# Kernel tuning notes

Hardware: AMD Instinct MI355X
Metric: run time of the kernel (lower is better)

The kernel has to match this reference:

```python
import jax, jax.numpy as jnp
import numpy as np

VOCAB, VEC, HID, ATT, DOM, B, S = 50000, 300, 256, 500, 16, 64, 128


def _gru_scan(gi_all, h0, Whh, bhh):
    # gi_all: [S,B,3H] precomputed input projections; returns hs: [S,B,H]
    def step(h, gi):
        gh = h @ Whh.T + bhh
        i_r, i_z, i_n = jnp.split(gi, 3, axis=-1)
        h_r, h_z, h_n = jnp.split(gh, 3, axis=-1)
        r = jax.nn.sigmoid(i_r + h_r)
        zg = jax.nn.sigmoid(i_z + h_z)
        n = jnp.tanh(i_n + r * h_n)
        h_new = (1.0 - zg) * n + zg * h
        return h_new, h_new
    _, hs = jax.lax.scan(step, h0, gi_all)
    return hs


def setup_inputs() -> dict:
    key = jax.random.key(0)
    ks = jax.random.split(key, 16)
    def xavier(k, shape):
        fan_in, fan_out = shape[-1], shape[0]
        std = float(np.sqrt(2.0 / (fan_in + fan_out)))
        return jax.random.normal(k, shape, dtype=jnp.float32) * std
    inp = {
        'x': jax.random.randint(ks[0], (B, S), 0, VOCAB),
        'z': jax.random.randint(ks[1], (B,), 0, DOM),
        'emb': jax.random.normal(ks[2], (VOCAB, VEC), dtype=jnp.float32) * 0.1,
        'Wih_f': xavier(ks[3], (3 * HID, VEC)),
        'Whh_f': xavier(ks[4], (3 * HID, HID)),
        'bih_f': jnp.zeros((3 * HID,), jnp.float32),
        'bhh_f': jnp.zeros((3 * HID,), jnp.float32),
        'Wih_b': xavier(ks[5], (3 * HID, VEC)),
        'Whh_b': xavier(ks[6], (3 * HID, HID)),
        'bih_b': jnp.zeros((3 * HID,), jnp.float32),
        'bhh_b': jnp.zeros((3 * HID,), jnp.float32),
        'att_fc_W': xavier(ks[7], (ATT, 2 * HID)),
        'att_fc_b': jnp.zeros((ATT,), jnp.float32),
        'att_weight': xavier(ks[8], (DOM, ATT)),
        'fc_W': xavier(ks[9], (2, 2 * HID)),
        'fc_b': jnp.zeros((2,), jnp.float32),
    }
    return inp


def reference(x, z, emb, Wih_f, Whh_f, bih_f, bhh_f, Wih_b, Whh_b, bih_b, bhh_b,
              att_fc_W, att_fc_b, att_weight, fc_W, fc_b):
    xe = emb[x]                              # [B,S,VEC]
    xs = jnp.transpose(xe, (1, 0, 2))        # [S,B,VEC] (seq-major like torch GRU)
    h0 = jnp.zeros((x.shape[0], HID), jnp.float32)
    gi_f = jnp.einsum('sbv,gv->sbg', xs, Wih_f) + bih_f
    hs_f = _gru_scan(gi_f, h0, Whh_f, bhh_f)                       # [S,B,H]
    gi_b = jnp.einsum('sbv,gv->sbg', xs[::-1], Wih_b) + bih_b
    hs_b = _gru_scan(gi_b, h0, Whh_b, bhh_b)[::-1]                 # [S,B,H]
    h = jnp.transpose(jnp.concatenate([hs_f, hs_b], axis=-1), (1, 0, 2))  # [B,S,2H]
    hr = jnp.tanh(jnp.einsum('bsh,ah->bsa', h, att_fc_W) + att_fc_b)      # [B,S,ATT]
    # batched gather of per-domain attention vector, then per-row dot
    u = jnp.einsum('bsa,ba->bs', hr, att_weight[z])                        # [B,S]
    att = jax.nn.softmax(u, axis=1)                                        # [B,S]
    pooled = jnp.einsum('bsh,bs->bh', h, att)                              # [B,2H]
    # dropout is identity in eval mode
    return pooled @ fc_W.T + fc_b                                          # [B,2]
```

## Files before the change

kernel.cpp:

```cpp
#include <hip/hip_runtime.h>
#include <math.h>

#define VEC   300
#define HID   256
#define ATT   500
#define NB    64
#define NS    128
#define G3    768
#define GIC   1536
#define H2    512

typedef _Float16 half1;
typedef _Float16 h2_t  __attribute__((ext_vector_type(2)));
typedef _Float16 f16x8 __attribute__((ext_vector_type(8)));
typedef float    f32x4 __attribute__((ext_vector_type(4)));

struct __align__(16) H8 { h2_t a, b, c, d; };

#if __has_builtin(__builtin_amdgcn_exp2f)
#define EXP2F(x) __builtin_amdgcn_exp2f(x)
#else
#define EXP2F(x) exp2f(x)
#endif
#if __has_builtin(__builtin_amdgcn_rcpf)
#define RCPF(x) __builtin_amdgcn_rcpf(x)
#else
#define RCPF(x) (1.0f/(x))
#endif

__device__ __forceinline__ float sigm(float x){ return RCPF(1.f + EXP2F(-1.44269504f*x)); }
__device__ __forceinline__ float tanh_fast(float x){ return 1.f - 2.f*RCPF(1.f + EXP2F(2.88539008f*x)); }

#if __has_builtin(__builtin_amdgcn_fdot2)
#define FDOT(w,h,acc) __builtin_amdgcn_fdot2((w),(h),(acc),false)
#else
#define FDOT(w,h,acc) ((acc) + (float)(w).x*(float)(h).x + (float)(w).y*(float)(h).y)
#endif

__global__ __launch_bounds__(256) void k_prep(const float* __restrict__ Wf,
                       const float* __restrict__ Wb, h2_t* __restrict__ Wpk){
  int o = blockIdx.x*256 + threadIdx.x;
  int t = o & 1023;
  int rest = o >> 10;
  int j = rest % 3;
  int p = (rest/3) & 31;
  int dir = rest / 96;
  int u = t & 255, ks = t >> 8;
  const float* W = dir ? Wb : Wf;
  int k0 = ks*64 + 2*p;
  h2_t w;
  w.x = (half1)W[(j*HID+u)*HID + k0];
  w.y = (half1)W[(j*HID+u)*HID + k0 + 1];
  Wpk[o] = w;
}

__global__ __launch_bounds__(256) void k_prepA(const float* __restrict__ afW,
                       half1* __restrict__ afW16){
  int o = blockIdx.x*256 + threadIdx.x;
  int n = o >> 9, k = o & 511;
  afW16[o] = (half1)((n < ATT) ? afW[n*H2 + k] : 0.f);
}

__global__ __launch_bounds__(256)
__attribute__((amdgpu_waves_per_eu(4, 4)))
void k_gi_mfma(const int* __restrict__ x,
      const float* __restrict__ emb,
      const float* __restrict__ Wf, const float* __restrict__ Wb,
      const float* __restrict__ bf, const float* __restrict__ bb,
      float* __restrict__ gi){
  __shared__ half1 Al[128*40];
  __shared__ half1 Bl[128*40];
  __shared__ int   xi[128];
  const int t = threadIdx.x;
  const int row0 = blockIdx.x * 128;
  const int col0 = blockIdx.y * 128;
  if (t < 128) {
    int i = row0 + t; int s = i >> 6; int b = i & 63;
    xi[t] = x[b*NS + s];
  }
  __syncthreads();

  const int lane = t & 63, wid = t >> 6;
  const int wr = wid >> 1, wc = wid & 1;
  const int l15 = lane & 15, lk = lane >> 4;

  f32x4 acc[4][4];
#pragma unroll
  for (int i = 0; i < 4; ++i)
#pragma unroll
    for (int j = 0; j < 4; ++j) acc[i][j] = (f32x4){0.f,0.f,0.f,0.f};

  for (int ks = 0; ks < 10; ++ks) {
#pragma unroll
    for (int l = 0; l < 8; ++l) {
      int idx = l*256 + t;
      int row = idx >> 4;
      int kp  = idx & 15;
      int kk  = ks*32 + kp*2;
      h2_t va; va.x = (half1)0.f; va.y = (half1)0.f;
      h2_t vb; vb.x = (half1)0.f; vb.y = (half1)0.f;
      if (kk < VEC) {
        float2 e = *reinterpret_cast<const float2*>(&emb[(long)xi[row]*VEC + kk]);
        va.x = (half1)e.x; va.y = (half1)e.y;
        int g = col0 + row;
        const float* W = (g < G3) ? &Wf[(long)g*VEC] : &Wb[(long)(g-G3)*VEC];
        float2 w2 = *reinterpret_cast<const float2*>(&W[kk]);
        vb.x = (half1)w2.x; vb.y = (half1)w2.y;
      }
      *reinterpret_cast<h2_t*>(&Al[row*40 + kp*2]) = va;
      *reinterpret_cast<h2_t*>(&Bl[row*40 + kp*2]) = vb;
    }
    __syncthreads();
    f16x8 af[4], bfq[4];
#pragma unroll
    for (int i = 0; i < 4; ++i)
      af[i]  = *reinterpret_cast<const f16x8*>(&Al[(wr*64 + i*16 + l15)*40 + lk*8]);
#pragma unroll
    for (int j = 0; j < 4; ++j)
      bfq[j] = *reinterpret_cast<const f16x8*>(&Bl[(wc*64 + j*16 + l15)*40 + lk*8]);
#pragma unroll
    for (int i = 0; i < 4; ++i)
#pragma unroll
      for (int j = 0; j < 4; ++j)
        acc[i][j] = __builtin_amdgcn_mfma_f32_16x16x32_f16(af[i], bfq[j], acc[i][j], 0, 0, 0);
    __syncthreads();
  }

#pragma unroll
  for (int j = 0; j < 4; ++j) {
    int gcol = col0 + wc*64 + j*16 + l15;
    float bj = (gcol < G3) ? bf[gcol] : bb[gcol - G3];
#pragma unroll
    for (int i = 0; i < 4; ++i) {
      int grow0 = row0 + wr*64 + i*16 + lk*4;
#pragma unroll
      for (int q = 0; q < 4; ++q)
        gi[(long)(grow0 + q)*GIC + gcol] = acc[i][j][q] + bj;
    }
  }
}

#define DECL12(X,g,UNUSED) h2_t X##g##a0,X##g##a1,X##g##a2, X##g##b0,X##g##b1,X##g##b2, \
                                X##g##c0,X##g##c1,X##g##c2, X##g##d0,X##g##d1,X##g##d2;
#define LOAD12(X,g,WP) \
  X##g##a0=(WP)[((4*(g)+0)*3+0)*1024]; X##g##a1=(WP)[((4*(g)+0)*3+1)*1024]; X##g##a2=(WP)[((4*(g)+0)*3+2)*1024]; \
  X##g##b0=(WP)[((4*(g)+1)*3+0)*1024]; X##g##b1=(WP)[((4*(g)+1)*3+1)*1024]; X##g##b2=(WP)[((4*(g)+1)*3+2)*1024]; \
  X##g##c0=(WP)[((4*(g)+2)*3+0)*1024]; X##g##c1=(WP)[((4*(g)+2)*3+1)*1024]; X##g##c2=(WP)[((4*(g)+2)*3+2)*1024]; \
  X##g##d0=(WP)[((4*(g)+3)*3+0)*1024]; X##g##d1=(WP)[((4*(g)+3)*3+1)*1024]; X##g##d2=(WP)[((4*(g)+3)*3+2)*1024];
#define FMA12(X,g,BOFF) { \
  H8 hv = *reinterpret_cast<const H8*>(&hr[kb + (BOFF) + (g)*8]); \
  a0=FDOT(X##g##a0,hv.a,a0); a1=FDOT(X##g##a1,hv.a,a1); a2=FDOT(X##g##a2,hv.a,a2); \
  a0=FDOT(X##g##b0,hv.b,a0); a1=FDOT(X##g##b1,hv.b,a1); a2=FDOT(X##g##b2,hv.b,a2); \
  a0=FDOT(X##g##c0,hv.c,a0); a1=FDOT(X##g##c1,hv.c,a1); a2=FDOT(X##g##c2,hv.c,a2); \
  a0=FDOT(X##g##d0,hv.d,a0); a1=FDOT(X##g##d1,hv.d,a1); a2=FDOT(X##g##d2,hv.d,a2); }
#define GRP8(M,X,A2) M(X,0,A2) M(X,1,A2) M(X,2,A2) M(X,3,A2) M(X,4,A2) M(X,5,A2) M(X,6,A2) M(X,7,A2)

__global__ __launch_bounds__(512)
__attribute__((amdgpu_waves_per_eu(2, 2)))
void k_scan_reg5(const float* __restrict__ gi,
     const h2_t* __restrict__ Wpk,
     const float* __restrict__ bhf, const float* __restrict__ bhb,
     float* __restrict__ hseq){
  __shared__ __align__(16) half1 hist[129*256];
  __shared__ float part[3*256];
  const int t   = threadIdx.x;
  const int u   = t & 255;
  const int ks  = t >> 8;
  const int kb  = ks * 128;
  const int dir = blockIdx.x & 1;
  const int b   = blockIdx.x >> 1;
  const float* bhh = dir ? bhb : bhf;
  const h2_t* wpA = Wpk + (long)dir*96*1024 + (2*ks)*256 + u;
  const h2_t* wpB = Wpk + (long)dir*96*1024 + (2*ks+1)*256 + u;

  GRP8(DECL12, A, 0)
  GRP8(DECL12, B, 0)
  GRP8(LOAD12, A, wpA)
  GRP8(LOAD12, B, wpB)

  float bh0=0.f, bh1=0.f, bh2=0.f;
  if (ks == 0) { bh0 = bhh[u]; bh1 = bhh[HID+u]; bh2 = bhh[2*HID+u]; }
  if (t < 256) hist[t] = (half1)0.f;
  float hprev = 0.f;
  __syncthreads();

#pragma unroll 1
  for (int tt = 0; tt < NS; ++tt) {
    const int s = dir ? (NS-1-tt) : tt;
    float i0=0.f, i1=0.f, i2=0.f;
    if (ks == 0) {
      long base = ((long)s*NB + b)*GIC + dir*G3 + u;
      i0 = gi[base]; i1 = gi[base+HID]; i2 = gi[base+2*HID];
    }
    const half1* hr = &hist[tt*256];
    float a0=0.f, a1=0.f, a2=0.f;
    GRP8(FMA12, A, 0)
    GRP8(FMA12, B, 64)
    if (ks == 1) { part[u] = a0; part[256+u] = a1; part[512+u] = a2; }
    __syncthreads();
    if (ks == 0) {
      float g0 = bh0 + a0 + part[u];
      float g1 = bh1 + a1 + part[256+u];
      float g2 = bh2 + a2 + part[512+u];
      float r  = sigm(i0 + g0);
      float zg = sigm(i1 + g1);
      float n  = tanh_fast(i2 + r*g2);
      float hn = (1.f - zg)*n + zg*hprev;
      hprev = hn;
      hist[(tt+1)*256 + u] = (half1)hn;
    }
    __syncthreads();
  }

#pragma unroll 1
  for (int it = 0; it < 16; ++it) {
    int idx = it*512 + t;
    int ttr = idx >> 6;
    int c4  = (idx & 63) * 4;
    int s   = dir ? (NS-1-ttr) : ttr;
    h2_t p0 = *reinterpret_cast<const h2_t*>(&hist[(ttr+1)*256 + c4]);
    h2_t p1 = *reinterpret_cast<const h2_t*>(&hist[(ttr+1)*256 + c4 + 2]);
    float4 v; v.x = (float)p0.x; v.y = (float)p0.y; v.z = (float)p1.x; v.w = (float)p1.y;
    *reinterpret_cast<float4*>(&hseq[((long)b*NS + s)*H2 + dir*HID + c4]) = v;
  }
}

__global__ __launch_bounds__(256)
__attribute__((amdgpu_waves_per_eu(4, 4)))
void k_att1_mfma(const float* __restrict__ hseq, const half1* __restrict__ afW16,
    const float* __restrict__ afb, const float* __restrict__ attw,
    const int* __restrict__ z, float* __restrict__ ub){
  __shared__ half1 Ah[32*520];
  __shared__ float red[4*32];
  const int t  = threadIdx.x;
  const int b  = blockIdx.x;
  const int s0 = blockIdx.y * 32;
  const int lane = t & 63, w = t >> 6;
  const int l15 = lane & 15, lk = lane >> 4;

#pragma unroll
  for (int l = 0; l < 64; ++l) {
    int idx = l*256 + t;
    int sl = idx >> 9, c = idx & 511;
    Ah[sl*520 + c] = (half1)hseq[((long)b*NS + s0 + sl)*H2 + c];
  }
  __syncthreads();

  f32x4 acc[2][8];
#pragma unroll
  for (int i = 0; i < 2; ++i)
#pragma unroll
    for (int j = 0; j < 8; ++j) acc[i][j] = (f32x4){0.f,0.f,0.f,0.f};

#pragma unroll 2
  for (int ksn = 0; ksn < 16; ++ksn) {
    f16x8 af[2];
#pragma unroll
    for (int mt = 0; mt < 2; ++mt)
      af[mt] = *reinterpret_cast<const f16x8*>(&Ah[(mt*16 + l15)*520 + ksn*32 + lk*8]);
#pragma unroll
    for (int nt = 0; nt < 8; ++nt) {
      int n = w*128 + nt*16 + l15;
      f16x8 bf = *reinterpret_cast<const f16x8*>(&afW16[(long)n*512 + ksn*32 + lk*8]);
#pragma unroll
      for (int mt = 0; mt < 2; ++mt)
        acc[mt][nt] = __builtin_amdgcn_mfma_f32_16x16x32_f16(af[mt], bf, acc[mt][nt], 0, 0, 0);
    }
  }

  float us[8];
#pragma unroll
  for (int i = 0; i < 8; ++i) us[i] = 0.f;
  const int zb = z[b];
#pragma unroll
  for (int nt = 0; nt < 8; ++nt) {
    int n = w*128 + nt*16 + l15;
    float ab = (n < ATT) ? afb[n] : 0.f;
    float aw = (n < ATT) ? attw[zb*ATT + n] : 0.f;
#pragma unroll
    for (int mt = 0; mt < 2; ++mt)
#pragma unroll
      for (int q = 0; q < 4; ++q)
        us[mt*4+q] += tanh_fast(acc[mt][nt][q] + ab) * aw;
  }
#pragma unroll
  for (int off = 1; off < 16; off <<= 1)
#pragma unroll
    for (int i = 0; i < 8; ++i) us[i] += __shfl_xor(us[i], off, 64);
  if (l15 == 0) {
#pragma unroll
    for (int i = 0; i < 8; ++i) {
      int row = (i >> 2)*16 + lk*4 + (i & 3);
      red[w*32 + row] = us[i];
    }
  }
  __syncthreads();
  if (t < 32)
    ub[b*NS + s0 + t] = red[t] + red[32+t] + red[64+t] + red[96+t];
}

__global__ __launch_bounds__(256) void k_att2(const float* __restrict__ hseq,
   const float* __restrict__ ub, const float* __restrict__ fcW,
   const float* __restrict__ fcb, float* __restrict__ out){
  __shared__ float att[NS];
  __shared__ float red[256];
  __shared__ float pool[H2];
  const int t = threadIdx.x, b = blockIdx.x;
  float v = (t < NS) ? ub[b*NS + t] : -3.4e38f;
  red[t] = v; __syncthreads();
  for (int off = 128; off >= 1; off >>= 1) {
    if (t < off) red[t] = fmaxf(red[t], red[t+off]);
    __syncthreads();
  }
  float mx = red[0]; __syncthreads();
  float e = (t < NS) ? EXP2F(1.44269504f*(v - mx)) : 0.f;
  red[t] = e; __syncthreads();
  for (int off = 128; off >= 1; off >>= 1) {
    if (t < off) red[t] += red[t+off];
    __syncthreads();
  }
  float sm = red[0]; __syncthreads();
  if (t < NS) att[t] = e / sm;
  __syncthreads();
#pragma unroll
  for (int rep = 0; rep < 2; ++rep) {
    int c = rep*256 + t;
    float acc = 0.f;
#pragma unroll 4
    for (int s = 0; s < NS; ++s) acc += att[s] * hseq[((long)b*NS + s)*H2 + c];
    pool[c] = acc;
  }
  __syncthreads();
  for (int j = 0; j < 2; ++j) {
    float p = pool[t]*fcW[j*H2+t] + pool[t+256]*fcW[j*H2+t+256];
    red[t] = p; __syncthreads();
    for (int off = 128; off >= 1; off >>= 1) {
      if (t < off) red[t] += red[t+off];
      __syncthreads();
    }
    if (t == 0) out[b*2+j] = red[0] + fcb[j];
    __syncthreads();
  }
}

extern "C" void kernel_launch(void* const* d_in, const int* in_sizes, int n_in,
                              void* d_out, int out_size, void* d_ws, size_t ws_size,
                              hipStream_t stream) {
  const int*   x     = (const int*)  d_in[0];
  const int*   z     = (const int*)  d_in[1];
  const float* emb   = (const float*)d_in[2];
  const float* Wih_f = (const float*)d_in[3];
  const float* Whh_f = (const float*)d_in[4];
  const float* bih_f = (const float*)d_in[5];
  const float* bhh_f = (const float*)d_in[6];
  const float* Wih_b = (const float*)d_in[7];
  const float* Whh_b = (const float*)d_in[8];
  const float* bih_b = (const float*)d_in[9];
  const float* bhh_b = (const float*)d_in[10];
  const float* afW   = (const float*)d_in[11];
  const float* afb   = (const float*)d_in[12];
  const float* attw  = (const float*)d_in[13];
  const float* fcW   = (const float*)d_in[14];
  const float* fcb   = (const float*)d_in[15];

  float* ws    = (float*)d_ws;
  h2_t*  Wpk   = (h2_t*)ws;
  half1* afW16 = (half1*)(ws + 196608);
  float* giW   = ws   + 196608 + 131072;
  float* hseq  = giW  + 12582912;
  float* ubuf  = hseq + 4194304;

  k_prep <<<dim3(768),  dim3(256), 0, stream>>>(Whh_f, Whh_b, Wpk);
  k_prepA<<<dim3(1024), dim3(256), 0, stream>>>(afW, afW16);
  k_gi_mfma<<<dim3(64,12), dim3(256), 0, stream>>>(x, emb, Wih_f, Wih_b, bih_f, bih_b, giW);
  k_scan_reg5<<<dim3(128), dim3(512), 0, stream>>>(giW, Wpk, bhh_f, bhh_b, hseq);
  k_att1_mfma<<<dim3(64,4), dim3(256), 0, stream>>>(hseq, afW16, afb, attw, z, ubuf);
  k_att2<<<dim3(64), dim3(256), 0, stream>>>(hseq, ubuf, fcW, fcb, (float*)d_out);
}
```

Baseline: 236.3 us.

## Reduce GRU split-K via wave shuffle and fuse attention kernels into one

The recurrent scan now places both K-halves of a hidden unit in the same wavefront, with lanes 0-31 and 32-63 holding the two halves. Partial sums are combined with a cross-lane xor shuffle instead of a shared-memory exchange, which removes one block barrier per timestep. The weight pre-pack is re-laid-out to match. Separately, the attention-score and softmax/pooling kernels are merged into one 512-thread block per batch row that keeps the whole sequence in LDS as fp16. This drops a launch and a global round trip, but only 64 blocks of parallelism are left for the attention MFMA work, and pooling now reads fp16 copies of the hidden states.

```diff
diff --git a/kernel.cpp b/kernel.cpp
--- a/kernel.cpp
+++ b/kernel.cpp
@@ -37,17 +37,18 @@
 #define FDOT(w,h,acc) ((acc) + (float)(w).x*(float)(h).x + (float)(w).y*(float)(h).y)
 #endif
 
-__global__ __launch_bounds__(256) void k_prep(const float* __restrict__ Wf,
+__global__ __launch_bounds__(256) void k_prep2(const float* __restrict__ Wf,
                        const float* __restrict__ Wb, h2_t* __restrict__ Wpk){
   int o = blockIdx.x*256 + threadIdx.x;
-  int t = o & 1023;
-  int rest = o >> 10;
+  int t = o & 511;
+  int rest = o >> 9;
   int j = rest % 3;
-  int p = (rest/3) & 31;
-  int dir = rest / 96;
-  int u = t & 255, ks = t >> 8;
+  int p = (rest/3) & 63;
+  int dir = rest / 192;
+  int u = (t >> 6)*32 + (t & 31);
+  int ks = (t >> 5) & 1;
   const float* W = dir ? Wb : Wf;
-  int k0 = ks*64 + 2*p;
+  int k0 = ks*128 + 2*p;
   h2_t w;
   w.x = (half1)W[(j*HID+u)*HID + k0];
   w.y = (half1)W[(j*HID+u)*HID + k0 + 1];
@@ -142,13 +143,13 @@
 
 #define DECL12(X,g,UNUSED) h2_t X##g##a0,X##g##a1,X##g##a2, X##g##b0,X##g##b1,X##g##b2, \
                                 X##g##c0,X##g##c1,X##g##c2, X##g##d0,X##g##d1,X##g##d2;
-#define LOAD12(X,g,WP) \
-  X##g##a0=(WP)[((4*(g)+0)*3+0)*1024]; X##g##a1=(WP)[((4*(g)+0)*3+1)*1024]; X##g##a2=(WP)[((4*(g)+0)*3+2)*1024]; \
-  X##g##b0=(WP)[((4*(g)+1)*3+0)*1024]; X##g##b1=(WP)[((4*(g)+1)*3+1)*1024]; X##g##b2=(WP)[((4*(g)+1)*3+2)*1024]; \
-  X##g##c0=(WP)[((4*(g)+2)*3+0)*1024]; X##g##c1=(WP)[((4*(g)+2)*3+1)*1024]; X##g##c2=(WP)[((4*(g)+2)*3+2)*1024]; \
-  X##g##d0=(WP)[((4*(g)+3)*3+0)*1024]; X##g##d1=(WP)[((4*(g)+3)*3+1)*1024]; X##g##d2=(WP)[((4*(g)+3)*3+2)*1024];
+#define LOAD12(X,g,PB) \
+  X##g##a0=wp[(((PB)+4*(g)+0)*3+0)*512]; X##g##a1=wp[(((PB)+4*(g)+0)*3+1)*512]; X##g##a2=wp[(((PB)+4*(g)+0)*3+2)*512]; \
+  X##g##b0=wp[(((PB)+4*(g)+1)*3+0)*512]; X##g##b1=wp[(((PB)+4*(g)+1)*3+1)*512]; X##g##b2=wp[(((PB)+4*(g)+1)*3+2)*512]; \
+  X##g##c0=wp[(((PB)+4*(g)+2)*3+0)*512]; X##g##c1=wp[(((PB)+4*(g)+2)*3+1)*512]; X##g##c2=wp[(((PB)+4*(g)+2)*3+2)*512]; \
+  X##g##d0=wp[(((PB)+4*(g)+3)*3+0)*512]; X##g##d1=wp[(((PB)+4*(g)+3)*3+1)*512]; X##g##d2=wp[(((PB)+4*(g)+3)*3+2)*512];
 #define FMA12(X,g,BOFF) { \
-  H8 hv = *reinterpret_cast<const H8*>(&hr[kb + (BOFF) + (g)*8]); \
+  H8 hv = *reinterpret_cast<const H8*>(&hr[(BOFF) + (g)*8]); \
   a0=FDOT(X##g##a0,hv.a,a0); a1=FDOT(X##g##a1,hv.a,a1); a2=FDOT(X##g##a2,hv.a,a2); \
   a0=FDOT(X##g##b0,hv.b,a0); a1=FDOT(X##g##b1,hv.b,a1); a2=FDOT(X##g##b2,hv.b,a2); \
   a0=FDOT(X##g##c0,hv.c,a0); a1=FDOT(X##g##c1,hv.c,a1); a2=FDOT(X##g##c2,hv.c,a2); \
@@ -157,51 +158,55 @@
 
 __global__ __launch_bounds__(512)
 __attribute__((amdgpu_waves_per_eu(2, 2)))
-void k_scan_reg5(const float* __restrict__ gi,
+void k_scan_reg6(const float* __restrict__ gi,
      const h2_t* __restrict__ Wpk,
      const float* __restrict__ bhf, const float* __restrict__ bhb,
      float* __restrict__ hseq){
   __shared__ __align__(16) half1 hist[129*256];
-  __shared__ float part[3*256];
-  const int t   = threadIdx.x;
-  const int u   = t & 255;
-  const int ks  = t >> 8;
-  const int kb  = ks * 128;
-  const int dir = blockIdx.x & 1;
-  const int b   = blockIdx.x >> 1;
+  const int t    = threadIdx.x;
+  const int lane = t & 63;
+  const int ul   = lane & 31;
+  const int ks   = lane >> 5;
+  const int w    = t >> 6;
+  const int u    = w*32 + ul;
+  const int ks128 = ks * 128;
+  const int dir  = blockIdx.x & 1;
+  const int b    = blockIdx.x >> 1;
   const float* bhh = dir ? bhb : bhf;
-  const h2_t* wpA = Wpk + (long)dir*96*1024 + (2*ks)*256 + u;
-  const h2_t* wpB = Wpk + (long)dir*96*1024 + (2*ks+1)*256 + u;
+  const h2_t* wp = Wpk + (long)dir*98304 + t;
 
   GRP8(DECL12, A, 0)
   GRP8(DECL12, B, 0)
-  GRP8(LOAD12, A, wpA)
-  GRP8(LOAD12, B, wpB)
-
+  GRP8(LOAD12, A, 0)
+  GRP8(LOAD12, B, 32)
+
+  const bool fin = (ks == 0);
   float bh0=0.f, bh1=0.f, bh2=0.f;
-  if (ks == 0) { bh0 = bhh[u]; bh1 = bhh[HID+u]; bh2 = bhh[2*HID+u]; }
+  if (fin) { bh0 = bhh[u]; bh1 = bhh[HID+u]; bh2 = bhh[2*HID+u]; }
   if (t < 256) hist[t] = (half1)0.f;
   float hprev = 0.f;
+
+  const long gstep = dir ? -(long)NB*GIC : (long)NB*GIC;
+  long gbase = ((long)(dir ? (NS-1) : 0)*NB + b)*GIC + dir*G3 + u;
   __syncthreads();
 
 #pragma unroll 1
   for (int tt = 0; tt < NS; ++tt) {
-    const int s = dir ? (NS-1-tt) : tt;
     float i0=0.f, i1=0.f, i2=0.f;
-    if (ks == 0) {
-      long base = ((long)s*NB + b)*GIC + dir*G3 + u;
-      i0 = gi[base]; i1 = gi[base+HID]; i2 = gi[base+2*HID];
-    }
-    const half1* hr = &hist[tt*256];
+    if (fin) {
+      i0 = gi[gbase]; i1 = gi[gbase+HID]; i2 = gi[gbase+2*HID];
+    }
+    const half1* hr = &hist[tt*256 + ks128];
     float a0=0.f, a1=0.f, a2=0.f;
     GRP8(FMA12, A, 0)
     GRP8(FMA12, B, 64)
-    if (ks == 1) { part[u] = a0; part[256+u] = a1; part[512+u] = a2; }
-    __syncthreads();
-    if (ks == 0) {
-      float g0 = bh0 + a0 + part[u];
-      float g1 = bh1 + a1 + part[256+u];
-      float g2 = bh2 + a2 + part[512+u];
+    a0 += __shfl_xor(a0, 32, 64);
+    a1 += __shfl_xor(a1, 32, 64);
+    a2 += __shfl_xor(a2, 32, 64);
+    if (fin) {
+      float g0 = bh0 + a0;
+      float g1 = bh1 + a1;
+      float g2 = bh2 + a2;
       float r  = sigm(i0 + g0);
       float zg = sigm(i1 + g1);
       float n  = tanh_fast(i2 + r*g2);
@@ -209,6 +214,7 @@
       hprev = hn;
       hist[(tt+1)*256 + u] = (half1)hn;
     }
+    gbase += gstep;
     __syncthreads();
   }
 
@@ -225,116 +231,94 @@
   }
 }
 
-__global__ __launch_bounds__(256)
-__attribute__((amdgpu_waves_per_eu(4, 4)))
-void k_att1_mfma(const float* __restrict__ hseq, const half1* __restrict__ afW16,
+__global__ __launch_bounds__(512)
+void k_att12(const float* __restrict__ hseq, const half1* __restrict__ afW16,
     const float* __restrict__ afb, const float* __restrict__ attw,
-    const int* __restrict__ z, float* __restrict__ ub){
-  __shared__ half1 Ah[32*520];
-  __shared__ float red[4*32];
+    const int* __restrict__ z, const float* __restrict__ fcW,
+    const float* __restrict__ fcb, float* __restrict__ out){
+  __shared__ half1 ht[128*520];
+  __shared__ float usl[NS];
+  __shared__ float att[NS];
+  __shared__ float red[512];
   const int t  = threadIdx.x;
   const int b  = blockIdx.x;
-  const int s0 = blockIdx.y * 32;
   const int lane = t & 63, w = t >> 6;
   const int l15 = lane & 15, lk = lane >> 4;
 
-#pragma unroll
-  for (int l = 0; l < 64; ++l) {
-    int idx = l*256 + t;
+#pragma unroll 4
+  for (int l = 0; l < 128; ++l) {
+    int idx = l*512 + t;
     int sl = idx >> 9, c = idx & 511;
-    Ah[sl*520 + c] = (half1)hseq[((long)b*NS + s0 + sl)*H2 + c];
-  }
-  __syncthreads();
-
-  f32x4 acc[2][8];
-#pragma unroll
-  for (int i = 0; i < 2; ++i)
-#pragma unroll
-    for (int j = 0; j < 8; ++j) acc[i][j] = (f32x4){0.f,0.f,0.f,0.f};
-
+    ht[sl*520 + c] = (half1)hseq[((long)b*NS + sl)*H2 + c];
+  }
+  __syncthreads();
+
+  const int zb = z[b];
+  float us[4];
+#pragma unroll
+  for (int q = 0; q < 4; ++q) us[q] = 0.f;
+
+#pragma unroll 1
+  for (int nc = 0; nc < 8; ++nc) {
+    f32x4 acc[4];
+#pragma unroll
+    for (int nf = 0; nf < 4; ++nf) acc[nf] = (f32x4){0.f,0.f,0.f,0.f};
 #pragma unroll 2
-  for (int ksn = 0; ksn < 16; ++ksn) {
-    f16x8 af[2];
-#pragma unroll
-    for (int mt = 0; mt < 2; ++mt)
-      af[mt] = *reinterpret_cast<const f16x8*>(&Ah[(mt*16 + l15)*520 + ksn*32 + lk*8]);
-#pragma unroll
-    for (int nt = 0; nt < 8; ++nt) {
-      int n = w*128 + nt*16 + l15;
-      f16x8 bf = *reinterpret_cast<const f16x8*>(&afW16[(long)n*512 + ksn*32 + lk*8]);
-#pragma unroll
-      for (int mt = 0; mt < 2; ++mt)
-        acc[mt][nt] = __builtin_amdgcn_mfma_f32_16x16x32_f16(af[mt], bf, acc[mt][nt], 0, 0, 0);
-    }
-  }
-
-  float us[8];
-#pragma unroll
-  for (int i = 0; i < 8; ++i) us[i] = 0.f;
-  const int zb = z[b];
-#pragma unroll
-  for (int nt = 0; nt < 8; ++nt) {
-    int n = w*128 + nt*16 + l15;
-    float ab = (n < ATT) ? afb[n] : 0.f;
-    float aw = (n < ATT) ? attw[zb*ATT + n] : 0.f;
-#pragma unroll
-    for (int mt = 0; mt < 2; ++mt)
+    for (int ksn = 0; ksn < 16; ++ksn) {
+      f16x8 af = *reinterpret_cast<const f16x8*>(&ht[(w*16 + l15)*520 + ksn*32 + lk*8]);
+#pragma unroll
+      for (int nf = 0; nf < 4; ++nf) {
+        int n = nc*64 + nf*16 + l15;
+        f16x8 bf = *reinterpret_cast<const f16x8*>(&afW16[(long)n*512 + ksn*32 + lk*8]);
+        acc[nf] = __builtin_amdgcn_mfma_f32_16x16x32_f16(af, bf, acc[nf], 0, 0, 0);
+      }
+    }
+#pragma unroll
+    for (int nf = 0; nf < 4; ++nf) {
+      int n = nc*64 + nf*16 + l15;
+      float ab = (n < ATT) ? afb[n] : 0.f;
+      float aw = (n < ATT) ? attw[zb*ATT + n] : 0.f;
 #pragma unroll
       for (int q = 0; q < 4; ++q)
-        us[mt*4+q] += tanh_fast(acc[mt][nt][q] + ab) * aw;
+        us[q] += tanh_fast(acc[nf][q] + ab) * aw;
+    }
   }
 #pragma unroll
   for (int off = 1; off < 16; off <<= 1)
 #pragma unroll
-    for (int i = 0; i < 8; ++i) us[i] += __shfl_xor(us[i], off, 64);
+    for (int q = 0; q < 4; ++q) us[q] += __shfl_xor(us[q], off, 64);
   if (l15 == 0) {
 #pragma unroll
-    for (int i = 0; i < 8; ++i) {
-      int row = (i >> 2)*16 + lk*4 + (i & 3);
-      red[w*32 + row] = us[i];
-    }
-  }
-  __syncthreads();
-  if (t < 32)
-    ub[b*NS + s0 + t] = red[t] + red[32+t] + red[64+t] + red[96+t];
-}
-
-__global__ __launch_bounds__(256) void k_att2(const float* __restrict__ hseq,
-   const float* __restrict__ ub, const float* __restrict__ fcW,
-   const float* __restrict__ fcb, float* __restrict__ out){
-  __shared__ float att[NS];
-  __shared__ float red[256];
-  __shared__ float pool[H2];
-  const int t = threadIdx.x, b = blockIdx.x;
-  float v = (t < NS) ? ub[b*NS + t] : -3.4e38f;
+    for (int q = 0; q < 4; ++q)
+      usl[w*16 + lk*4 + q] = us[q];
+  }
+  __syncthreads();
+
+  float v = (t < NS) ? usl[t] : -3.4e38f;
   red[t] = v; __syncthreads();
-  for (int off = 128; off >= 1; off >>= 1) {
-    if (t < off) red[t] = fmaxf(red[t], red[t+off]);
+  for (int off = 256; off >= 1; off >>= 1) {
+    if (t < off && t + off < 512) red[t] = fmaxf(red[t], red[t+off]);
     __syncthreads();
   }
   float mx = red[0]; __syncthreads();
   float e = (t < NS) ? EXP2F(1.44269504f*(v - mx)) : 0.f;
   red[t] = e; __syncthreads();
-  for (int off = 128; off >= 1; off >>= 1) {
-    if (t < off) red[t] += red[t+off];
+  for (int off = 256; off >= 1; off >>= 1) {
+    if (t < off && t + off < 512) red[t] += red[t+off];
     __syncthreads();
   }
   float sm = red[0]; __syncthreads();
   if (t < NS) att[t] = e / sm;
   __syncthreads();
-#pragma unroll
-  for (int rep = 0; rep < 2; ++rep) {
-    int c = rep*256 + t;
-    float acc = 0.f;
+
+  float p = 0.f;
 #pragma unroll 4
-    for (int s = 0; s < NS; ++s) acc += att[s] * hseq[((long)b*NS + s)*H2 + c];
-    pool[c] = acc;
-  }
-  __syncthreads();
+  for (int s = 0; s < NS; ++s)
+    p += att[s] * (float)ht[s*520 + t];
+
   for (int j = 0; j < 2; ++j) {
-    float p = pool[t]*fcW[j*H2+t] + pool[t+256]*fcW[j*H2+t+256];
-    red[t] = p; __syncthreads();
-    for (int off = 128; off >= 1; off >>= 1) {
+    red[t] = p * fcW[j*H2 + t]; __syncthreads();
+    for (int off = 256; off >= 1; off >>= 1) {
       if (t < off) red[t] += red[t+off];
       __syncthreads();
     }
@@ -368,12 +352,10 @@
   half1* afW16 = (half1*)(ws + 196608);
   float* giW   = ws   + 196608 + 131072;
   float* hseq  = giW  + 12582912;
-  float* ubuf  = hseq + 4194304;
-
-  k_prep <<<dim3(768),  dim3(256), 0, stream>>>(Whh_f, Whh_b, Wpk);
+
+  k_prep2<<<dim3(768),  dim3(256), 0, stream>>>(Whh_f, Whh_b, Wpk);
   k_prepA<<<dim3(1024), dim3(256), 0, stream>>>(afW, afW16);
   k_gi_mfma<<<dim3(64,12), dim3(256), 0, stream>>>(x, emb, Wih_f, Wih_b, bih_f, bih_b, giW);
-  k_scan_reg5<<<dim3(128), dim3(512), 0, stream>>>(giW, Wpk, bhh_f, bhh_b, hseq);
-  k_att1_mfma<<<dim3(64,4), dim3(256), 0, stream>>>(hseq, afW16, afb, attw, z, ubuf);
-  k_att2<<<dim3(64), dim3(256), 0, stream>>>(hseq, ubuf, fcW, fcb, (float*)d_out);
-}
+  k_scan_reg6<<<dim3(128), dim3(512), 0, stream>>>(giW, Wpk, bhh_f, bhh_b, hseq);
+  k_att12<<<dim3(64), dim3(512), 0, stream>>>(hseq, afW16, afb, attw, z, fcW, fcb, (float*)d_out);
+}
```

Result: slower. 338.0 us (+43.1%).

## Split GRU k-halves within a wavefront and reduce with shuffles instead of LDS

Applied to the files above, without the earlier changes.

Remaps the scan kernel's threads so the two k-halves for each hidden unit sit in the same wavefront, 32 lanes apart. Weights are repacked to match. Partial gate sums are then combined with cross-lane xor shuffles rather than written to shared memory. This removes one __syncthreads and the LDS round trip from every one of the 128 sequential steps. It also strength-reduces the gi address computation. In exchange, half of each wavefront idles during the gate math, and the history reads are now split across lanes within a wave.

```diff
diff --git a/kernel.cpp b/kernel.cpp
--- a/kernel.cpp
+++ b/kernel.cpp
@@ -37,17 +37,18 @@
 #define FDOT(w,h,acc) ((acc) + (float)(w).x*(float)(h).x + (float)(w).y*(float)(h).y)
 #endif
 
-__global__ __launch_bounds__(256) void k_prep(const float* __restrict__ Wf,
+__global__ __launch_bounds__(256) void k_prep2(const float* __restrict__ Wf,
                        const float* __restrict__ Wb, h2_t* __restrict__ Wpk){
   int o = blockIdx.x*256 + threadIdx.x;
-  int t = o & 1023;
-  int rest = o >> 10;
+  int t = o & 511;
+  int rest = o >> 9;
   int j = rest % 3;
-  int p = (rest/3) & 31;
-  int dir = rest / 96;
-  int u = t & 255, ks = t >> 8;
+  int p = (rest/3) & 63;
+  int dir = rest / 192;
+  int u = (t >> 6)*32 + (t & 31);
+  int ks = (t >> 5) & 1;
   const float* W = dir ? Wb : Wf;
-  int k0 = ks*64 + 2*p;
+  int k0 = ks*128 + 2*p;
   h2_t w;
   w.x = (half1)W[(j*HID+u)*HID + k0];
   w.y = (half1)W[(j*HID+u)*HID + k0 + 1];
@@ -142,13 +143,13 @@
 
 #define DECL12(X,g,UNUSED) h2_t X##g##a0,X##g##a1,X##g##a2, X##g##b0,X##g##b1,X##g##b2, \
                                 X##g##c0,X##g##c1,X##g##c2, X##g##d0,X##g##d1,X##g##d2;
-#define LOAD12(X,g,WP) \
-  X##g##a0=(WP)[((4*(g)+0)*3+0)*1024]; X##g##a1=(WP)[((4*(g)+0)*3+1)*1024]; X##g##a2=(WP)[((4*(g)+0)*3+2)*1024]; \
-  X##g##b0=(WP)[((4*(g)+1)*3+0)*1024]; X##g##b1=(WP)[((4*(g)+1)*3+1)*1024]; X##g##b2=(WP)[((4*(g)+1)*3+2)*1024]; \
-  X##g##c0=(WP)[((4*(g)+2)*3+0)*1024]; X##g##c1=(WP)[((4*(g)+2)*3+1)*1024]; X##g##c2=(WP)[((4*(g)+2)*3+2)*1024]; \
-  X##g##d0=(WP)[((4*(g)+3)*3+0)*1024]; X##g##d1=(WP)[((4*(g)+3)*3+1)*1024]; X##g##d2=(WP)[((4*(g)+3)*3+2)*1024];
+#define LOAD12(X,g,PB) \
+  X##g##a0=wp[(((PB)+4*(g)+0)*3+0)*512]; X##g##a1=wp[(((PB)+4*(g)+0)*3+1)*512]; X##g##a2=wp[(((PB)+4*(g)+0)*3+2)*512]; \
+  X##g##b0=wp[(((PB)+4*(g)+1)*3+0)*512]; X##g##b1=wp[(((PB)+4*(g)+1)*3+1)*512]; X##g##b2=wp[(((PB)+4*(g)+1)*3+2)*512]; \
+  X##g##c0=wp[(((PB)+4*(g)+2)*3+0)*512]; X##g##c1=wp[(((PB)+4*(g)+2)*3+1)*512]; X##g##c2=wp[(((PB)+4*(g)+2)*3+2)*512]; \
+  X##g##d0=wp[(((PB)+4*(g)+3)*3+0)*512]; X##g##d1=wp[(((PB)+4*(g)+3)*3+1)*512]; X##g##d2=wp[(((PB)+4*(g)+3)*3+2)*512];
 #define FMA12(X,g,BOFF) { \
-  H8 hv = *reinterpret_cast<const H8*>(&hr[kb + (BOFF) + (g)*8]); \
+  H8 hv = *reinterpret_cast<const H8*>(&hr[(BOFF) + (g)*8]); \
   a0=FDOT(X##g##a0,hv.a,a0); a1=FDOT(X##g##a1,hv.a,a1); a2=FDOT(X##g##a2,hv.a,a2); \
   a0=FDOT(X##g##b0,hv.b,a0); a1=FDOT(X##g##b1,hv.b,a1); a2=FDOT(X##g##b2,hv.b,a2); \
   a0=FDOT(X##g##c0,hv.c,a0); a1=FDOT(X##g##c1,hv.c,a1); a2=FDOT(X##g##c2,hv.c,a2); \
@@ -157,51 +158,55 @@
 
 __global__ __launch_bounds__(512)
 __attribute__((amdgpu_waves_per_eu(2, 2)))
-void k_scan_reg5(const float* __restrict__ gi,
+void k_scan_reg6(const float* __restrict__ gi,
      const h2_t* __restrict__ Wpk,
      const float* __restrict__ bhf, const float* __restrict__ bhb,
      float* __restrict__ hseq){
   __shared__ __align__(16) half1 hist[129*256];
-  __shared__ float part[3*256];
-  const int t   = threadIdx.x;
-  const int u   = t & 255;
-  const int ks  = t >> 8;
-  const int kb  = ks * 128;
-  const int dir = blockIdx.x & 1;
-  const int b   = blockIdx.x >> 1;
+  const int t    = threadIdx.x;
+  const int lane = t & 63;
+  const int ul   = lane & 31;
+  const int ks   = lane >> 5;
+  const int w    = t >> 6;
+  const int u    = w*32 + ul;
+  const int ks128 = ks * 128;
+  const int dir  = blockIdx.x & 1;
+  const int b    = blockIdx.x >> 1;
   const float* bhh = dir ? bhb : bhf;
-  const h2_t* wpA = Wpk + (long)dir*96*1024 + (2*ks)*256 + u;
-  const h2_t* wpB = Wpk + (long)dir*96*1024 + (2*ks+1)*256 + u;
+  const h2_t* wp = Wpk + (long)dir*98304 + t;
 
   GRP8(DECL12, A, 0)
   GRP8(DECL12, B, 0)
-  GRP8(LOAD12, A, wpA)
-  GRP8(LOAD12, B, wpB)
-
+  GRP8(LOAD12, A, 0)
+  GRP8(LOAD12, B, 32)
+
+  const bool fin = (ks == 0);
   float bh0=0.f, bh1=0.f, bh2=0.f;
-  if (ks == 0) { bh0 = bhh[u]; bh1 = bhh[HID+u]; bh2 = bhh[2*HID+u]; }
+  if (fin) { bh0 = bhh[u]; bh1 = bhh[HID+u]; bh2 = bhh[2*HID+u]; }
   if (t < 256) hist[t] = (half1)0.f;
   float hprev = 0.f;
+
+  const long gstep = dir ? -(long)NB*GIC : (long)NB*GIC;
+  long gbase = ((long)(dir ? (NS-1) : 0)*NB + b)*GIC + dir*G3 + u;
   __syncthreads();
 
 #pragma unroll 1
   for (int tt = 0; tt < NS; ++tt) {
-    const int s = dir ? (NS-1-tt) : tt;
     float i0=0.f, i1=0.f, i2=0.f;
-    if (ks == 0) {
-      long base = ((long)s*NB + b)*GIC + dir*G3 + u;
-      i0 = gi[base]; i1 = gi[base+HID]; i2 = gi[base+2*HID];
-    }
-    const half1* hr = &hist[tt*256];
+    if (fin) {
+      i0 = gi[gbase]; i1 = gi[gbase+HID]; i2 = gi[gbase+2*HID];
+    }
+    const half1* hr = &hist[tt*256 + ks128];
     float a0=0.f, a1=0.f, a2=0.f;
     GRP8(FMA12, A, 0)
     GRP8(FMA12, B, 64)
-    if (ks == 1) { part[u] = a0; part[256+u] = a1; part[512+u] = a2; }
-    __syncthreads();
-    if (ks == 0) {
-      float g0 = bh0 + a0 + part[u];
-      float g1 = bh1 + a1 + part[256+u];
-      float g2 = bh2 + a2 + part[512+u];
+    a0 += __shfl_xor(a0, 32, 64);
+    a1 += __shfl_xor(a1, 32, 64);
+    a2 += __shfl_xor(a2, 32, 64);
+    if (fin) {
+      float g0 = bh0 + a0;
+      float g1 = bh1 + a1;
+      float g2 = bh2 + a2;
       float r  = sigm(i0 + g0);
       float zg = sigm(i1 + g1);
       float n  = tanh_fast(i2 + r*g2);
@@ -209,6 +214,7 @@
       hprev = hn;
       hist[(tt+1)*256 + u] = (half1)hn;
     }
+    gbase += gstep;
     __syncthreads();
   }
 
@@ -370,10 +376,10 @@
   float* hseq  = giW  + 12582912;
   float* ubuf  = hseq + 4194304;
 
-  k_prep <<<dim3(768),  dim3(256), 0, stream>>>(Whh_f, Whh_b, Wpk);
+  k_prep2<<<dim3(768),  dim3(256), 0, stream>>>(Whh_f, Whh_b, Wpk);
   k_prepA<<<dim3(1024), dim3(256), 0, stream>>>(afW, afW16);
   k_gi_mfma<<<dim3(64,12), dim3(256), 0, stream>>>(x, emb, Wih_f, Wih_b, bih_f, bih_b, giW);
-  k_scan_reg5<<<dim3(128), dim3(512), 0, stream>>>(giW, Wpk, bhh_f, bhh_b, hseq);
+  k_scan_reg6<<<dim3(128), dim3(512), 0, stream>>>(giW, Wpk, bhh_f, bhh_b, hseq);
   k_att1_mfma<<<dim3(64,4), dim3(256), 0, stream>>>(hseq, afW16, afb, attw, z, ubuf);
   k_att2<<<dim3(64), dim3(256), 0, stream>>>(hseq, ubuf, fcW, fcb, (float*)d_out);
 }
```

Result: no change. 233.7 us (median of 2 runs) (-1.1%).
